# Kernel optimization log

Measured on AMD Instinct MI355X. Metric: run time of the kernel, lower is better.

The kernel has to match this reference:

```python
import jax, jax.numpy as jnp
import numpy as np

B = 16384
STATE = 524   # state_dim / output_size
IENC = 256    # INet output dim
ZD = 32       # z_dim
H = 256       # expert hidden size
E = 5         # num_experts
HG = 256      # gating hidden size
IN1 = STATE + IENC + ZD   # 812, PredictionNet layer-1 input
IN2 = H + ZD              # 288, layers 2/3 input


def _uni(k, shape):
    # matches PredictionNet.init_params glorot-style uniform bound
    bound = float(np.sqrt(6.0 / (shape[-2] * shape[-1])))
    return jax.random.uniform(k, shape, jnp.float32, -bound, bound)


def setup_inputs() -> dict:
    key = jax.random.key(0)
    ks = jax.random.split(key, 12)
    d = {}
    d['z'] = jax.random.normal(ks[0], (B, ZD), jnp.float32)
    d['p_prev'] = jax.random.normal(ks[1], (B, STATE), jnp.float32)
    d['I'] = jax.random.normal(ks[2], (B, 2048), jnp.float32)
    # gating network: (state+z) -> HG -> HG//2 -> E
    d['gw1'] = _uni(ks[3], (STATE + ZD, HG)); d['gb1'] = jnp.zeros((HG,), jnp.float32)
    d['gw2'] = _uni(ks[4], (HG, HG // 2));    d['gb2'] = jnp.zeros((HG // 2,), jnp.float32)
    d['gw3'] = _uni(ks[5], (HG // 2, E));     d['gb3'] = jnp.zeros((E,), jnp.float32)
    # INet: 2048 -> 256 -> 256 -> 256
    d['iw1'] = _uni(ks[6], (2048, IENC)); d['ib1'] = jnp.zeros((IENC,), jnp.float32)
    d['iw2'] = _uni(ks[7], (IENC, IENC)); d['ib2'] = jnp.zeros((IENC,), jnp.float32)
    d['iw3'] = _uni(ks[8], (IENC, IENC)); d['ib3'] = jnp.zeros((IENC,), jnp.float32)
    # expert weights [E, in, out], biases [E, out]
    d['w_l1'] = _uni(ks[9], (E, IN1, H));     d['b_l1'] = jnp.zeros((E, H), jnp.float32)
    d['w_l2'] = _uni(ks[10], (E, IN2, H));    d['b_l2'] = jnp.zeros((E, H), jnp.float32)
    d['w_l3'] = _uni(ks[11], (E, IN2, STATE)); d['b_l3'] = jnp.zeros((E, STATE), jnp.float32)
    return d


def reference(z, p_prev, I, gw1, gb1, gw2, gb2, gw3, gb3,
              iw1, ib1, iw2, ib2, iw3, ib3,
              w_l1, b_l1, w_l2, b_l2, w_l3, b_l3):
    elu = jax.nn.elu
    # gating network -> softmax blending coefficients omega [B, E]
    g = elu(jnp.concatenate([z, p_prev], axis=1) @ gw1 + gb1)
    g = elu(g @ gw2 + gb2)
    omega = jax.nn.softmax(g @ gw3 + gb3, axis=-1)
    # interaction encoder
    Ienc = elu(elu(elu(I @ iw1 + ib1) @ iw2 + ib2) @ iw3 + ib3)
    x = jnp.concatenate([p_prev, Ienc], axis=1)  # [B, STATE+IENC]

    def moe_linear(h, W, b):
        # same math as sum_e omega_e * (h @ W_e) + omega @ b, without
        # materializing per-sample blended [B, in, out] weights
        per_expert = jnp.einsum('bi,eio->beo', h, W)
        return jnp.einsum('be,beo->bo', omega, per_expert) + omega @ b

    h0 = jnp.concatenate([z, x], axis=1)          # [B, 812]
    h1 = elu(moe_linear(h0, w_l1, b_l1))          # [B, 256]
    h2 = elu(moe_linear(jnp.concatenate([z, h1], axis=1), w_l2, b_l2))
    h3 = moe_linear(jnp.concatenate([z, h2], axis=1), w_l3, b_l3)  # [B, 524]
    return h3
```

## Files before the change

kernel.cpp:

```cpp
#include <hip/hip_runtime.h>
#include <hip/hip_bf16.h>
#include <cstdint>
#include <cstddef>


#define BATCH 16384

typedef __attribute__((ext_vector_type(8))) short short8;
typedef __attribute__((ext_vector_type(4))) float f32x4;
typedef unsigned short u16;
typedef unsigned int u32;

typedef __attribute__((address_space(3))) void lds_t;
typedef __attribute__((address_space(1))) void gmem_t;

__device__ __forceinline__ void gload16(const u16* g, u16* l) {
  __builtin_amdgcn_global_load_lds((gmem_t*)(u16*)g, (lds_t*)l, 16, 0, 0);
}

__device__ __forceinline__ float bf2f(u16 u) {
  union { float f; u32 i; } v; v.i = ((u32)u) << 16; return v.f;
}
__device__ __forceinline__ u16 f2bf(float f) {
  union { float f; u32 i; } v; v.f = f;
  u32 x = v.i;
  return (u16)((x + 0x7fffu + ((x >> 16) & 1u)) >> 16);
}
__device__ __forceinline__ u16 load_bf(const void* p, long i, int f32) {
  return f32 ? f2bf(((const float*)p)[i]) : ((const u16*)p)[i];
}
__device__ __forceinline__ float elu_f(float x) { return x > 0.f ? x : expm1f(x); }

__device__ __forceinline__ int swz(int row, int q) { return q ^ ((row >> 1) & 3); }

__global__ __launch_bounds__(256) void detect_dtype(const u32* __restrict__ zr,
                                                    int* __restrict__ flag)
{
  __shared__ int cnt;
  if (threadIdx.x == 0) cnt = 0;
  __syncthreads();
  u32 w = zr[threadIdx.x];
  int e = (w >> 7) & 0xFF;
  if (e >= 112 && e <= 142) atomicAdd(&cnt, 1);
  __syncthreads();
  if (threadIdx.x == 0) *flag = (cnt < 128) ? 1 : 0;
}

__global__ __launch_bounds__(256) void prep_kernel(
    const void* __restrict__ z, const void* __restrict__ p,
    const int* __restrict__ flagp,
    u16* __restrict__ h0, u16* __restrict__ h1c, u16* __restrict__ h2c,
    const void* ib1, const void* ib2, const void* ib3,
    const void* gb1, const void* gb2, const void* gb3,
    const void* gw3, const void* bl1, const void* bl2, const void* bl3,
    u16* __restrict__ smallc)
{
  const int f32 = *flagp;
  const int b = blockIdx.y;
  const int c = blockIdx.x * 256 + threadIdx.x;
  if (blockIdx.y == 0 && blockIdx.x == 0) {
    for (long j = threadIdx.x; j < 7100; j += 256) {
      u16 v;
      if      (j < 256)  v = load_bf(ib1, j,        f32);
      else if (j < 512)  v = load_bf(ib2, j - 256,  f32);
      else if (j < 768)  v = load_bf(ib3, j - 512,  f32);
      else if (j < 1024) v = load_bf(gb1, j - 768,  f32);
      else if (j < 1152) v = load_bf(gb2, j - 1024, f32);
      else if (j < 1280) v = (j - 1152 < 5) ? load_bf(gb3, j - 1152, f32) : (u16)0;
      else if (j < 1920) v = load_bf(gw3, j - 1280, f32);
      else if (j < 3200) v = load_bf(bl1, j - 1920, f32);
      else if (j < 4480) v = load_bf(bl2, j - 3200, f32);
      else               v = load_bf(bl3, j - 4480, f32);
      smallc[j] = v;
    }
  }
  if (c >= 832) return;
  const long i = (long)b * 832 + c;
  if (c < 32) {
    u16 v = load_bf(z, (long)b * 32 + c, f32);
    h0[i] = v;
    h1c[(long)b * 288 + c] = v;
    h2c[(long)b * 288 + c] = v;
  } else if (c < 556) {
    h0[i] = load_bf(p, (long)b * 524 + (c - 32), f32);
  } else if (c >= 812) {
    h0[i] = 0;
  }
}

__global__ __launch_bounds__(256) void convert_I(
    const void* __restrict__ I, const int* __restrict__ flagp,
    u16* __restrict__ out)
{
  const int f32 = *flagp;
  const long total8 = (long)BATCH * 2048 / 8;
  const long stride = (long)gridDim.x * blockDim.x;
  for (long t = (long)blockIdx.x * blockDim.x + threadIdx.x; t < total8; t += stride) {
    if (f32) {
      const float4* src = (const float4*)I;
      float4 a = src[t * 2], b = src[t * 2 + 1];
      union { u16 r[8]; uint4 v; } u;
      u.r[0] = f2bf(a.x); u.r[1] = f2bf(a.y); u.r[2] = f2bf(a.z); u.r[3] = f2bf(a.w);
      u.r[4] = f2bf(b.x); u.r[5] = f2bf(b.y); u.r[6] = f2bf(b.z); u.r[7] = f2bf(b.w);
      *(uint4*)(out + t * 8) = u.v;
    } else {
      *(uint4*)(out + t * 8) = ((const uint4*)I)[t];
    }
  }
}

struct TPSeg { long end; int K, N, Kp, Np; };

__global__ __launch_bounds__(256) void transpose_all(
    const int* __restrict__ flagp,
    const void* s0, const void* s1, const void* s2, const void* s3,
    const void* s4, const void* s5, const void* s6, const void* s7,
    u16* d0, u16* d1, u16* d2, u16* d3, u16* d4, u16* d5, u16* d6, u16* d7)
{
  const TPSeg seg[8] = {
    {  524288, 2048, 256, 2048, 256 },
    {  589824,  256, 256,  256, 256 },
    {  655360,  256, 256,  256, 256 },
    {  802816,  556, 256,  576, 256 },
    {  835584,  256, 128,  256, 128 },
    { 1900544,  812, 256,  832, 256 },
    { 2269184,  288, 256,  288, 256 },
    { 3098624,  288, 524,  288, 576 },
  };
  const void* const srcs[8] = { s0, s1, s2, s3, s4, s5, s6, s7 };
  u16* const dsts[8] = { d0, d1, d2, d3, d4, d5, d6, d7 };
  const int f32 = *flagp;
  const long total = 3098624;
  const long stride = (long)gridDim.x * blockDim.x;
  for (long i = (long)blockIdx.x * blockDim.x + threadIdx.x; i < total; i += stride) {
    int s = 0;
    long base = 0;
    while (i >= seg[s].end) { base = seg[s].end; ++s; }
    const long j = i - base;
    const int Kp = seg[s].Kp, Np = seg[s].Np, K = seg[s].K, N = seg[s].N;
    const int k = (int)(j % Kp);
    const long t = j / Kp;
    const int n = (int)(t % Np);
    const int e = (int)(t / Np);
    u16 v = 0;
    if (k < K && n < N) v = load_bf(srcs[s], (long)e * K * N + (long)k * N + n, f32);
    dsts[s][j] = v;
  }
}

template<bool ELU>
__global__ __launch_bounds__(256, 2) void gemm64(
    const u16* __restrict__ A, int lda,
    const u16* __restrict__ Wt, int ldw,
    const u16* __restrict__ bias,
    u16* __restrict__ C, int ldc, int col_off, int K)
{
  __shared__ __align__(16) u16 sA[2][64 * 32];
  __shared__ __align__(16) u16 sB[2][128 * 32];

  const int tid  = threadIdx.x;
  const int bm   = blockIdx.x, bn = blockIdx.y;
  const int lane = tid & 63, wave = tid >> 6;
  const int wm = (wave & 1) * 32, wn = (wave >> 1) * 64;
  const int lrow = lane & 15, lq = lane >> 4;

  const int sq    = (lane & 3) ^ ((lane >> 3) & 3);
  const int srowA = 16 * wave + (lane >> 2);
  const int srowB = 32 * wave + (lane >> 2);
  const u16* Ag = A  + (size_t)(bm * 64  + srowA) * lda + sq * 8;
  const u16* Wg = Wt + (size_t)(bn * 128 + srowB) * ldw + sq * 8;
  const int laOff = wave * 512;
  const int lbOff = wave * 1024;

  f32x4 acc[2][4] = {};
  const int nt = K / 32;

  gload16(Ag, sA[0] + laOff);
  gload16(Wg, sB[0] + lbOff);
  gload16(Wg + (size_t)16 * ldw, sB[0] + lbOff + 512);
  __syncthreads();

  for (int t = 0; t < nt; ++t) {
    const int cur = t & 1;
    if (t + 1 < nt) {
      const int k0 = (t + 1) * 32;
      gload16(Ag + k0, sA[cur ^ 1] + laOff);
      gload16(Wg + k0, sB[cur ^ 1] + lbOff);
      gload16(Wg + (size_t)16 * ldw + k0, sB[cur ^ 1] + lbOff + 512);
    }

    short8 a[2], b[4];
#pragma unroll
    for (int i = 0; i < 2; ++i) {
      const int r = wm + i * 16 + lrow;
      a[i] = *(const short8*)(sA[cur] + r * 32 + swz(r, lq) * 8);
    }
#pragma unroll
    for (int i = 0; i < 4; ++i) {
      const int r = wn + i * 16 + lrow;
      b[i] = *(const short8*)(sB[cur] + r * 32 + swz(r, lq) * 8);
    }

#pragma unroll
    for (int mi = 0; mi < 2; ++mi)
#pragma unroll
      for (int ni = 0; ni < 4; ++ni)
        acc[mi][ni] = __builtin_amdgcn_mfma_f32_16x16x32_bf16(a[mi], b[ni], acc[mi][ni], 0, 0, 0);

    __syncthreads();
  }

#pragma unroll
  for (int ni = 0; ni < 4; ++ni) {
    const int col = bn * 128 + wn + ni * 16 + lrow;
    const float bv = bf2f(bias[col]);
#pragma unroll
    for (int mi = 0; mi < 2; ++mi) {
#pragma unroll
      for (int r = 0; r < 4; ++r) {
        const int row = bm * 64 + wm + mi * 16 + lq * 4 + r;
        float v = acc[mi][ni][r] + bv;
        if (ELU) v = elu_f(v);
        C[(size_t)row * ldc + col_off + col] = f2bf(v);
      }
    }
  }
}

__global__ __launch_bounds__(256) void gating3_kernel(
    const u16* __restrict__ g2, const u16* __restrict__ gw3c,
    const u16* __restrict__ gb3c, float* __restrict__ omega)
{
  const int wid  = (blockIdx.x << 2) + (threadIdx.x >> 6);
  const int lane = threadIdx.x & 63;
  const u32 gp = *(const u32*)(g2 + (size_t)wid * 128 + lane * 2);
  const float x0 = bf2f((u16)(gp & 0xffffu));
  const float x1 = bf2f((u16)(gp >> 16));
  float acc[5];
#pragma unroll
  for (int e = 0; e < 5; ++e)
    acc[e] = x0 * bf2f(gw3c[(lane * 2) * 5 + e]) + x1 * bf2f(gw3c[(lane * 2 + 1) * 5 + e]);
#pragma unroll
  for (int off = 1; off < 64; off <<= 1) {
#pragma unroll
    for (int e = 0; e < 5; ++e) acc[e] += __shfl_xor(acc[e], off);
  }
  if (lane == 0) {
    float t[5], m = -1e30f;
#pragma unroll
    for (int e = 0; e < 5; ++e) { t[e] = acc[e] + bf2f(gb3c[e]); m = fmaxf(m, t[e]); }
    float s = 0.f;
#pragma unroll
    for (int e = 0; e < 5; ++e) { t[e] = expf(t[e] - m); s += t[e]; }
    const float inv = 1.f / s;
#pragma unroll
    for (int e = 0; e < 5; ++e) omega[(size_t)wid * 5 + e] = t[e] * inv;
  }
}

template<bool ELU>
__global__ __launch_bounds__(256, 2) void moe_gemm(
    const u16* __restrict__ A, int lda,
    const u16* __restrict__ Wt, int ldw, long wstride_e,
    const u16* __restrict__ bias, int bias_n,
    const float* __restrict__ omega,
    void* __restrict__ C, int ldc, int col_off, int n_store, int K,
    const int* __restrict__ flagp, int is_final)
{
  __shared__ __align__(16) u16 sA[2][128 * 32];
  __shared__ __align__(16) u16 sW[2][5][64 * 32];
  __shared__ float som[128 * 5];
  __shared__ float sbias[5][64];

  const int tid  = threadIdx.x;
  const int bm   = blockIdx.x, bn = blockIdx.y;
  const int lane = tid & 63, wave = tid >> 6;
  const int wm = (wave & 1) * 64, wn = (wave >> 1) * 32;
  const int lrow = lane & 15, lq = lane >> 4;
  const int f32out = is_final ? *flagp : 0;

  const int sq = (lane & 3) ^ ((lane >> 3) & 3);
  const int srowA = 32 * wave + (lane >> 2);
  const int srowW = 16 * wave + (lane >> 2);
  const u16* Ag = A  + (size_t)(bm * 128 + srowA) * lda + sq * 8;
  const u16* Wg = Wt + (size_t)(bn * 64 + srowW) * ldw + sq * 8;
  const int laOff = wave * 1024;
  const int lWoff = wave * 512;

  f32x4 acc[5][4][2] = {};
  const int nt = K / 32;

  gload16(Ag, sA[0] + laOff);
  gload16(Ag + (size_t)16 * lda, sA[0] + laOff + 512);
#pragma unroll
  for (int e = 0; e < 5; ++e)
    gload16(Wg + e * wstride_e, sW[0][e] + lWoff);

  for (int t = tid; t < 960; t += 256) {
    if (t < 640) {
      som[t] = omega[(size_t)(bm * 128) * 5 + t];
    } else {
      const int j = t - 640;
      const int e = j >> 6, c = j & 63;
      const int col = bn * 64 + c;
      sbias[e][c] = (col < bias_n) ? bf2f(bias[(size_t)e * bias_n + col]) : 0.f;
    }
  }
  __syncthreads();

  for (int t = 0; t < nt; ++t) {
    const int cur = t & 1;
    if (t + 1 < nt) {
      const int k0 = (t + 1) * 32;
      gload16(Ag + k0, sA[cur ^ 1] + laOff);
      gload16(Ag + (size_t)16 * lda + k0, sA[cur ^ 1] + laOff + 512);
#pragma unroll
      for (int e = 0; e < 5; ++e)
        gload16(Wg + e * wstride_e + k0, sW[cur ^ 1][e] + lWoff);
    }

    short8 a[4];
#pragma unroll
    for (int i = 0; i < 4; ++i) {
      const int r = wm + i * 16 + lrow;
      a[i] = *(const short8*)(sA[cur] + r * 32 + swz(r, lq) * 8);
    }
    const int rb0 = wn + lrow, rb1 = rb0 + 16;
    const int ob0 = rb0 * 32 + swz(rb0, lq) * 8;
    const int ob1 = rb1 * 32 + swz(rb1, lq) * 8;
#pragma unroll
    for (int e = 0; e < 5; ++e) {
      short8 b0 = *(const short8*)(sW[cur][e] + ob0);
      short8 b1 = *(const short8*)(sW[cur][e] + ob1);
#pragma unroll
      for (int mi = 0; mi < 4; ++mi) {
        acc[e][mi][0] = __builtin_amdgcn_mfma_f32_16x16x32_bf16(a[mi], b0, acc[e][mi][0], 0, 0, 0);
        acc[e][mi][1] = __builtin_amdgcn_mfma_f32_16x16x32_bf16(a[mi], b1, acc[e][mi][1], 0, 0, 0);
      }
    }

    __syncthreads();
  }

#pragma unroll
  for (int mi = 0; mi < 4; ++mi) {
#pragma unroll
    for (int r = 0; r < 4; ++r) {
      const int rl = wm + mi * 16 + lq * 4 + r;
      const int row = bm * 128 + rl;
      float om[5];
#pragma unroll
      for (int e = 0; e < 5; ++e) om[e] = som[rl * 5 + e];
#pragma unroll
      for (int ni = 0; ni < 2; ++ni) {
        const int c = wn + ni * 16 + lrow;
        const int col = bn * 64 + c;
        if (col < n_store) {
          float v = 0.f;
#pragma unroll
          for (int e = 0; e < 5; ++e) v += om[e] * (acc[e][mi][ni][r] + sbias[e][c]);
          if (ELU) v = elu_f(v);
          const size_t idx = (size_t)row * ldc + col_off + col;
          if (f32out) ((float*)C)[idx] = v;
          else        ((u16*)C)[idx]   = f2bf(v);
        }
      }
    }
  }
}

extern "C" void kernel_launch(void* const* d_in, const int* in_sizes, int n_in,
                              void* d_out, int out_size, void* d_ws, size_t ws_size,
                              hipStream_t stream)
{
  const void* z    = d_in[0];
  const void* pprev= d_in[1];
  const void* I    = d_in[2];
  const void* gw1  = d_in[3];
  const void* gb1  = d_in[4];
  const void* gw2  = d_in[5];
  const void* gb2  = d_in[6];
  const void* gw3  = d_in[7];
  const void* gb3  = d_in[8];
  const void* iw1  = d_in[9];
  const void* ib1  = d_in[10];
  const void* iw2  = d_in[11];
  const void* ib2  = d_in[12];
  const void* iw3  = d_in[13];
  const void* ib3  = d_in[14];
  const void* wl1  = d_in[15];
  const void* bl1  = d_in[16];
  const void* wl2  = d_in[17];
  const void* bl2  = d_in[18];
  const void* wl3  = d_in[19];
  const void* bl3  = d_in[20];

  char* base = (char*)d_ws;
  size_t off = 0;
  auto alloc = [&](size_t bytes) -> void* {
    void* p = base + off;
    off = (off + bytes + 255) & ~(size_t)255;
    return p;
  };

  const size_t B = BATCH;
  int* flagp   = (int*)alloc(256);
  u16* h0      = (u16*)alloc(B * 832 * 2);
  u16* h1c     = (u16*)alloc(B * 288 * 2);
  u16* h2c     = (u16*)alloc(B * 288 * 2);
  u16* i1      = (u16*)alloc(B * 256 * 2);
  u16* i2      = (u16*)alloc(B * 256 * 2);
  float* omega = (float*)alloc(B * 5 * 4);
  u16* Ibf     = (u16*)alloc(B * 2048 * 2);
  u16* smallc  = (u16*)alloc(7100 * 2);
  u16* iw1t = (u16*)alloc((size_t)256 * 2048 * 2);
  u16* iw2t = (u16*)alloc((size_t)256 * 256 * 2);
  u16* iw3t = (u16*)alloc((size_t)256 * 256 * 2);
  u16* gw1t = (u16*)alloc((size_t)256 * 576 * 2);
  u16* gw2t = (u16*)alloc((size_t)128 * 256 * 2);
  u16* wl1t = (u16*)alloc((size_t)5 * 256 * 832 * 2);
  u16* wl2t = (u16*)alloc((size_t)5 * 256 * 288 * 2);
  u16* wl3t = (u16*)alloc((size_t)5 * 576 * 288 * 2);
  u16* g1 = i1;
  u16* g2 = i2;
  (void)in_sizes; (void)n_in; (void)out_size; (void)ws_size;

  u16* ib1c = smallc + 0,   *ib2c = smallc + 256, *ib3c = smallc + 512;
  u16* gb1c = smallc + 768, *gb2c = smallc + 1024, *gb3c = smallc + 1152;
  u16* gw3c = smallc + 1280;
  u16* bl1c = smallc + 1920, *bl2c = smallc + 3200, *bl3c = smallc + 4480;

  detect_dtype<<<1, 256, 0, stream>>>((const u32*)z, flagp);
  prep_kernel<<<dim3(4, BATCH), 256, 0, stream>>>(z, pprev, flagp, h0, h1c, h2c,
      ib1, ib2, ib3, gb1, gb2, gb3, gw3, bl1, bl2, bl3, smallc);
  convert_I<<<4096, 256, 0, stream>>>(I, flagp, Ibf);
  transpose_all<<<3072, 256, 0, stream>>>(flagp,
      iw1, iw2, iw3, gw1, gw2, wl1, wl2, wl3,
      iw1t, iw2t, iw3t, gw1t, gw2t, wl1t, wl2t, wl3t);

  gemm64<true><<<dim3(BATCH/64, 2), 256, 0, stream>>>(Ibf, 2048, iw1t, 2048, ib1c, i1, 256, 0,   2048);
  gemm64<true><<<dim3(BATCH/64, 2), 256, 0, stream>>>(i1,  256,  iw2t, 256,  ib2c, i2, 256, 0,   256);
  gemm64<true><<<dim3(BATCH/64, 2), 256, 0, stream>>>(i2,  256,  iw3t, 256,  ib3c, h0, 832, 556, 256);

  gemm64<true><<<dim3(BATCH/64, 2), 256, 0, stream>>>(h0, 832, gw1t, 576, gb1c, g1, 256, 0, 576);
  gemm64<true><<<dim3(BATCH/64, 1), 256, 0, stream>>>(g1, 256, gw2t, 256, gb2c, g2, 128, 0, 256);
  gating3_kernel<<<BATCH/4, 256, 0, stream>>>(g2, gw3c, gb3c, omega);

  moe_gemm<true><<<dim3(BATCH/128, 4), 256, 0, stream>>>(
      h0, 832, wl1t, 832, (long)256 * 832, bl1c, 256, omega, h1c, 288, 32, 256, 832, flagp, 0);
  moe_gemm<true><<<dim3(BATCH/128, 4), 256, 0, stream>>>(
      h1c, 288, wl2t, 288, (long)256 * 288, bl2c, 256, omega, h2c, 288, 32, 256, 288, flagp, 0);
  moe_gemm<false><<<dim3(BATCH/128, 9), 256, 0, stream>>>(
      h2c, 288, wl3t, 288, (long)576 * 288, bl3c, 524, omega, d_out, 524, 0, 524, 288, flagp, 1);
}
```

Measured before the change: 557.9 us.

## Fuse prep kernels, batch independent GEMMs, triple-buffer loads, and fold gating softmax into MoE

The four setup kernels become one prep_all kernel that detects the dtype per block via ballot, converts I, fills h0/h1c/h2c with 4-wide stores, and transposes weights four elements at a time. Independent INet and gating GEMMs are launched together through a two-descriptor gemm64m kernel, which also moves to a three-stage LDS pipeline with explicit vmcnt waits, non-draining barriers and raised MFMA priority. The gating layer-3 plus softmax is recomputed inside each MoE GEMM block, so the separate gating kernel and omega buffer go away. This cuts launch count and improves latency hiding, at the cost of redundant softmax work across column blocks, more LDS use, and fragile hand-written waitcnt logic.

```diff
diff --git a/kernel.cpp b/kernel.cpp
--- a/kernel.cpp
+++ b/kernel.cpp
@@ -18,6 +18,17 @@
   __builtin_amdgcn_global_load_lds((gmem_t*)(u16*)g, (lds_t*)l, 16, 0, 0);
 }
 
+__device__ __forceinline__ void barrier_nodrain() {
+  asm volatile("" ::: "memory");
+  __builtin_amdgcn_s_barrier();
+  asm volatile("" ::: "memory");
+}
+__device__ __forceinline__ void barrier_lds() {
+  asm volatile("s_waitcnt lgkmcnt(0)" ::: "memory");
+  __builtin_amdgcn_s_barrier();
+  asm volatile("" ::: "memory");
+}
+
 __device__ __forceinline__ float bf2f(u16 u) {
   union { float f; u32 i; } v; v.i = ((u32)u) << 16; return v.f;
 }
@@ -33,32 +44,33 @@
 
 __device__ __forceinline__ int swz(int row, int q) { return q ^ ((row >> 1) & 3); }
 
-__global__ __launch_bounds__(256) void detect_dtype(const u32* __restrict__ zr,
-                                                    int* __restrict__ flag)
-{
-  __shared__ int cnt;
-  if (threadIdx.x == 0) cnt = 0;
-  __syncthreads();
-  u32 w = zr[threadIdx.x];
-  int e = (w >> 7) & 0xFF;
-  if (e >= 112 && e <= 142) atomicAdd(&cnt, 1);
-  __syncthreads();
-  if (threadIdx.x == 0) *flag = (cnt < 128) ? 1 : 0;
-}
-
-__global__ __launch_bounds__(256) void prep_kernel(
+struct TPSeg { long end; int K, N, Kp, Np; };
+
+__global__ __launch_bounds__(256) void prep_all(
     const void* __restrict__ z, const void* __restrict__ p,
-    const int* __restrict__ flagp,
+    const void* __restrict__ I, int* __restrict__ flagp,
     u16* __restrict__ h0, u16* __restrict__ h1c, u16* __restrict__ h2c,
+    u16* __restrict__ Ibf,
     const void* ib1, const void* ib2, const void* ib3,
     const void* gb1, const void* gb2, const void* gb3,
     const void* gw3, const void* bl1, const void* bl2, const void* bl3,
-    u16* __restrict__ smallc)
+    u16* __restrict__ smallc,
+    const void* s0, const void* s1, const void* s2, const void* s3,
+    const void* s4, const void* s5, const void* s6, const void* s7,
+    u16* d0, u16* d1, u16* d2, u16* d3, u16* d4, u16* d5, u16* d6, u16* d7)
 {
-  const int f32 = *flagp;
-  const int b = blockIdx.y;
-  const int c = blockIdx.x * 256 + threadIdx.x;
-  if (blockIdx.y == 0 && blockIdx.x == 0) {
+  __shared__ int scnt[4];
+  {
+    u32 w = ((const u32*)z)[threadIdx.x];
+    int e = (w >> 7) & 0xFF;
+    unsigned long long m = __ballot(e >= 112 && e <= 142);
+    if ((threadIdx.x & 63) == 0) scnt[threadIdx.x >> 6] = __popcll(m);
+  }
+  __syncthreads();
+  const int f32 = (scnt[0] + scnt[1] + scnt[2] + scnt[3] < 128) ? 1 : 0;
+  if (blockIdx.x == 0 && threadIdx.x == 0) *flagp = f32;
+
+  if (blockIdx.x == 0) {
     for (long j = threadIdx.x; j < 7100; j += 256) {
       u16 v;
       if      (j < 256)  v = load_bf(ib1, j,        f32);
@@ -74,49 +86,7 @@
       smallc[j] = v;
     }
   }
-  if (c >= 832) return;
-  const long i = (long)b * 832 + c;
-  if (c < 32) {
-    u16 v = load_bf(z, (long)b * 32 + c, f32);
-    h0[i] = v;
-    h1c[(long)b * 288 + c] = v;
-    h2c[(long)b * 288 + c] = v;
-  } else if (c < 556) {
-    h0[i] = load_bf(p, (long)b * 524 + (c - 32), f32);
-  } else if (c >= 812) {
-    h0[i] = 0;
-  }
-}
-
-__global__ __launch_bounds__(256) void convert_I(
-    const void* __restrict__ I, const int* __restrict__ flagp,
-    u16* __restrict__ out)
-{
-  const int f32 = *flagp;
-  const long total8 = (long)BATCH * 2048 / 8;
-  const long stride = (long)gridDim.x * blockDim.x;
-  for (long t = (long)blockIdx.x * blockDim.x + threadIdx.x; t < total8; t += stride) {
-    if (f32) {
-      const float4* src = (const float4*)I;
-      float4 a = src[t * 2], b = src[t * 2 + 1];
-      union { u16 r[8]; uint4 v; } u;
-      u.r[0] = f2bf(a.x); u.r[1] = f2bf(a.y); u.r[2] = f2bf(a.z); u.r[3] = f2bf(a.w);
-      u.r[4] = f2bf(b.x); u.r[5] = f2bf(b.y); u.r[6] = f2bf(b.z); u.r[7] = f2bf(b.w);
-      *(uint4*)(out + t * 8) = u.v;
-    } else {
-      *(uint4*)(out + t * 8) = ((const uint4*)I)[t];
-    }
-  }
-}
-
-struct TPSeg { long end; int K, N, Kp, Np; };
-
-__global__ __launch_bounds__(256) void transpose_all(
-    const int* __restrict__ flagp,
-    const void* s0, const void* s1, const void* s2, const void* s3,
-    const void* s4, const void* s5, const void* s6, const void* s7,
-    u16* d0, u16* d1, u16* d2, u16* d3, u16* d4, u16* d5, u16* d6, u16* d7)
-{
+
   const TPSeg seg[8] = {
     {  524288, 2048, 256, 2048, 256 },
     {  589824,  256, 256,  256, 256 },
@@ -129,37 +99,94 @@
   };
   const void* const srcs[8] = { s0, s1, s2, s3, s4, s5, s6, s7 };
   u16* const dsts[8] = { d0, d1, d2, d3, d4, d5, d6, d7 };
-  const int f32 = *flagp;
-  const long total = 3098624;
+
+  const long NC = (long)BATCH * 2048 / 8;
+  const long NP = (long)BATCH * 208;
+  const long NT = 774656;
+  const long total = NC + NP + NT;
   const long stride = (long)gridDim.x * blockDim.x;
-  for (long i = (long)blockIdx.x * blockDim.x + threadIdx.x; i < total; i += stride) {
-    int s = 0;
-    long base = 0;
-    while (i >= seg[s].end) { base = seg[s].end; ++s; }
-    const long j = i - base;
-    const int Kp = seg[s].Kp, Np = seg[s].Np, K = seg[s].K, N = seg[s].N;
-    const int k = (int)(j % Kp);
-    const long t = j / Kp;
-    const int n = (int)(t % Np);
-    const int e = (int)(t / Np);
-    u16 v = 0;
-    if (k < K && n < N) v = load_bf(srcs[s], (long)e * K * N + (long)k * N + n, f32);
-    dsts[s][j] = v;
-  }
-}
-
-template<bool ELU>
-__global__ __launch_bounds__(256, 2) void gemm64(
-    const u16* __restrict__ A, int lda,
-    const u16* __restrict__ Wt, int ldw,
-    const u16* __restrict__ bias,
-    u16* __restrict__ C, int ldc, int col_off, int K)
+
+  for (long it = (long)blockIdx.x * 256 + threadIdx.x; it < total; it += stride) {
+    if (it < NC) {
+      const long t = it;
+      if (f32) {
+        const float4* src = (const float4*)I;
+        float4 a = src[t * 2], b = src[t * 2 + 1];
+        union { u16 r[8]; uint4 v; } u;
+        u.r[0] = f2bf(a.x); u.r[1] = f2bf(a.y); u.r[2] = f2bf(a.z); u.r[3] = f2bf(a.w);
+        u.r[4] = f2bf(b.x); u.r[5] = f2bf(b.y); u.r[6] = f2bf(b.z); u.r[7] = f2bf(b.w);
+        *(uint4*)(Ibf + t * 8) = u.v;
+      } else {
+        *(uint4*)(Ibf + t * 8) = ((const uint4*)I)[t];
+      }
+    } else if (it < NC + NP) {
+      const long j = it - NC;
+      const int b = (int)(j / 208);
+      const int c = (int)(j % 208) * 4;
+      ushort4 v;
+      if (c < 32) {
+        const long zi = (long)b * 32 + c;
+        if (f32) {
+          const float4 f = *(const float4*)((const float*)z + zi);
+          v.x = f2bf(f.x); v.y = f2bf(f.y); v.z = f2bf(f.z); v.w = f2bf(f.w);
+        } else {
+          v = *(const ushort4*)((const u16*)z + zi);
+        }
+        *(ushort4*)(h0 + (long)b * 832 + c) = v;
+        *(ushort4*)(h1c + (long)b * 288 + c) = v;
+        *(ushort4*)(h2c + (long)b * 288 + c) = v;
+      } else if (c < 556) {
+        const long pi = (long)b * 524 + (c - 32);
+        if (f32) {
+          const float4 f = *(const float4*)((const float*)p + pi);
+          v.x = f2bf(f.x); v.y = f2bf(f.y); v.z = f2bf(f.z); v.w = f2bf(f.w);
+        } else {
+          v = *(const ushort4*)((const u16*)p + pi);
+        }
+        *(ushort4*)(h0 + (long)b * 832 + c) = v;
+      } else {
+        v.x = 0; v.y = 0; v.z = 0; v.w = 0;
+        *(ushort4*)(h0 + (long)b * 832 + c) = v;
+      }
+    } else {
+      const long jd = (it - NC - NP) * 4;
+      int s = 0; long sbase = 0;
+      while (jd >= seg[s].end) { sbase = seg[s].end; ++s; }
+      const long jj = jd - sbase;
+      const int Kp = seg[s].Kp, Np = seg[s].Np, Kk = seg[s].K, Nn = seg[s].N;
+      const int k = (int)(jj % Kp);
+      const long tt = jj / Kp;
+      const int n = (int)(tt % Np);
+      const int e = (int)(tt / Np);
+      ushort4 v; v.x = 0; v.y = 0; v.z = 0; v.w = 0;
+      if (k < Kk && n < Nn) {
+        const long sb = (long)e * Kk * Nn + (long)k * Nn + n;
+        v.x = load_bf(srcs[s], sb, f32);
+        v.y = load_bf(srcs[s], sb + Nn, f32);
+        v.z = load_bf(srcs[s], sb + 2 * (long)Nn, f32);
+        v.w = load_bf(srcs[s], sb + 3 * (long)Nn, f32);
+      }
+      *(ushort4*)(dsts[s] + jj) = v;
+    }
+  }
+}
+
+struct GemmDesc {
+  const u16* A; const u16* Wt; const u16* bias; u16* C;
+  int lda, ldw, ldc, col_off, K, ny;
+};
+
+__global__ __launch_bounds__(256, 2) void gemm64m(GemmDesc da, GemmDesc db)
 {
-  __shared__ __align__(16) u16 sA[2][64 * 32];
-  __shared__ __align__(16) u16 sB[2][128 * 32];
+  __shared__ __align__(16) u16 sA[3][64 * 32];
+  __shared__ __align__(16) u16 sB[3][128 * 32];
+
+  int bn = blockIdx.y;
+  GemmDesc d;
+  if (bn < da.ny) { d = da; } else { bn -= da.ny; d = db; }
 
   const int tid  = threadIdx.x;
-  const int bm   = blockIdx.x, bn = blockIdx.y;
+  const int bm   = blockIdx.x;
   const int lane = tid & 63, wave = tid >> 6;
   const int wm = (wave & 1) * 32, wn = (wave >> 1) * 64;
   const int lrow = lane & 15, lq = lane >> 4;
@@ -167,27 +194,37 @@
   const int sq    = (lane & 3) ^ ((lane >> 3) & 3);
   const int srowA = 16 * wave + (lane >> 2);
   const int srowB = 32 * wave + (lane >> 2);
-  const u16* Ag = A  + (size_t)(bm * 64  + srowA) * lda + sq * 8;
-  const u16* Wg = Wt + (size_t)(bn * 128 + srowB) * ldw + sq * 8;
+  const u16* Ag = d.A  + (size_t)(bm * 64  + srowA) * d.lda + sq * 8;
+  const u16* Wg = d.Wt + (size_t)(bn * 128 + srowB) * d.ldw + sq * 8;
   const int laOff = wave * 512;
   const int lbOff = wave * 1024;
+  const int ldw = d.ldw;
 
   f32x4 acc[2][4] = {};
-  const int nt = K / 32;
+  const int nt = d.K / 32;
 
   gload16(Ag, sA[0] + laOff);
   gload16(Wg, sB[0] + lbOff);
   gload16(Wg + (size_t)16 * ldw, sB[0] + lbOff + 512);
-  __syncthreads();
+  gload16(Ag + 32, sA[1] + laOff);
+  gload16(Wg + 32, sB[1] + lbOff);
+  gload16(Wg + (size_t)16 * ldw + 32, sB[1] + lbOff + 512);
 
   for (int t = 0; t < nt; ++t) {
-    const int cur = t & 1;
-    if (t + 1 < nt) {
-      const int k0 = (t + 1) * 32;
-      gload16(Ag + k0, sA[cur ^ 1] + laOff);
-      gload16(Wg + k0, sB[cur ^ 1] + lbOff);
-      gload16(Wg + (size_t)16 * ldw + k0, sB[cur ^ 1] + lbOff + 512);
-    }
+    const int cur = t % 3;
+    barrier_nodrain();
+    if (t + 2 < nt) {
+      const int nb = (t + 2) % 3;
+      const int k0 = (t + 2) * 32;
+      gload16(Ag + k0, sA[nb] + laOff);
+      gload16(Wg + k0, sB[nb] + lbOff);
+      gload16(Wg + (size_t)16 * ldw + k0, sB[nb] + lbOff + 512);
+    }
+    const int ahead = nt - 1 - t;
+    if (ahead >= 2)      asm volatile("s_waitcnt vmcnt(6)" ::: "memory");
+    else if (ahead == 1) asm volatile("s_waitcnt vmcnt(3)" ::: "memory");
+    else                 asm volatile("s_waitcnt vmcnt(0)" ::: "memory");
+    barrier_nodrain();
 
     short8 a[2], b[4];
 #pragma unroll
@@ -201,60 +238,29 @@
       b[i] = *(const short8*)(sB[cur] + r * 32 + swz(r, lq) * 8);
     }
 
+    __builtin_amdgcn_s_setprio(1);
 #pragma unroll
     for (int mi = 0; mi < 2; ++mi)
 #pragma unroll
       for (int ni = 0; ni < 4; ++ni)
         acc[mi][ni] = __builtin_amdgcn_mfma_f32_16x16x32_bf16(a[mi], b[ni], acc[mi][ni], 0, 0, 0);
-
-    __syncthreads();
+    __builtin_amdgcn_s_setprio(0);
   }
 
 #pragma unroll
   for (int ni = 0; ni < 4; ++ni) {
     const int col = bn * 128 + wn + ni * 16 + lrow;
-    const float bv = bf2f(bias[col]);
+    const float bv = bf2f(d.bias[col]);
 #pragma unroll
     for (int mi = 0; mi < 2; ++mi) {
 #pragma unroll
       for (int r = 0; r < 4; ++r) {
         const int row = bm * 64 + wm + mi * 16 + lq * 4 + r;
         float v = acc[mi][ni][r] + bv;
-        if (ELU) v = elu_f(v);
-        C[(size_t)row * ldc + col_off + col] = f2bf(v);
-      }
-    }
-  }
-}
-
-__global__ __launch_bounds__(256) void gating3_kernel(
-    const u16* __restrict__ g2, const u16* __restrict__ gw3c,
-    const u16* __restrict__ gb3c, float* __restrict__ omega)
-{
-  const int wid  = (blockIdx.x << 2) + (threadIdx.x >> 6);
-  const int lane = threadIdx.x & 63;
-  const u32 gp = *(const u32*)(g2 + (size_t)wid * 128 + lane * 2);
-  const float x0 = bf2f((u16)(gp & 0xffffu));
-  const float x1 = bf2f((u16)(gp >> 16));
-  float acc[5];
-#pragma unroll
-  for (int e = 0; e < 5; ++e)
-    acc[e] = x0 * bf2f(gw3c[(lane * 2) * 5 + e]) + x1 * bf2f(gw3c[(lane * 2 + 1) * 5 + e]);
-#pragma unroll
-  for (int off = 1; off < 64; off <<= 1) {
-#pragma unroll
-    for (int e = 0; e < 5; ++e) acc[e] += __shfl_xor(acc[e], off);
-  }
-  if (lane == 0) {
-    float t[5], m = -1e30f;
-#pragma unroll
-    for (int e = 0; e < 5; ++e) { t[e] = acc[e] + bf2f(gb3c[e]); m = fmaxf(m, t[e]); }
-    float s = 0.f;
-#pragma unroll
-    for (int e = 0; e < 5; ++e) { t[e] = expf(t[e] - m); s += t[e]; }
-    const float inv = 1.f / s;
-#pragma unroll
-    for (int e = 0; e < 5; ++e) omega[(size_t)wid * 5 + e] = t[e] * inv;
+        v = elu_f(v);
+        d.C[(size_t)row * d.ldc + d.col_off + col] = f2bf(v);
+      }
+    }
   }
 }
 
@@ -263,14 +269,17 @@
     const u16* __restrict__ A, int lda,
     const u16* __restrict__ Wt, int ldw, long wstride_e,
     const u16* __restrict__ bias, int bias_n,
-    const float* __restrict__ omega,
+    const u16* __restrict__ g2, const u16* __restrict__ gw3c,
+    const u16* __restrict__ gb3c,
     void* __restrict__ C, int ldc, int col_off, int n_store, int K,
     const int* __restrict__ flagp, int is_final)
 {
   __shared__ __align__(16) u16 sA[2][128 * 32];
-  __shared__ __align__(16) u16 sW[2][5][64 * 32];
+  __shared__ __align__(16) u16 sW[2][5 * 64 * 32];
   __shared__ float som[128 * 5];
   __shared__ float sbias[5][64];
+  __shared__ float sgw[128 * 5];
+  __shared__ float sgb[5];
 
   const int tid  = threadIdx.x;
   const int bm   = blockIdx.x, bn = blockIdx.y;
@@ -287,37 +296,64 @@
   const int laOff = wave * 1024;
   const int lWoff = wave * 512;
 
+  auto stage = [&](int buf, int k0) {
+    gload16(Ag + k0, sA[buf] + laOff);
+    gload16(Ag + (size_t)16 * lda + k0, sA[buf] + laOff + 512);
+#pragma unroll
+    for (int e = 0; e < 5; ++e)
+      gload16(Wg + e * wstride_e + k0, sW[buf] + e * 2048 + lWoff);
+  };
+
   f32x4 acc[5][4][2] = {};
   const int nt = K / 32;
 
-  gload16(Ag, sA[0] + laOff);
-  gload16(Ag + (size_t)16 * lda, sA[0] + laOff + 512);
-#pragma unroll
-  for (int e = 0; e < 5; ++e)
-    gload16(Wg + e * wstride_e, sW[0][e] + lWoff);
-
-  for (int t = tid; t < 960; t += 256) {
-    if (t < 640) {
-      som[t] = omega[(size_t)(bm * 128) * 5 + t];
+  stage(0, 0);
+  for (int t2 = tid; t2 < 960; t2 += 256) {
+    if (t2 < 640) {
+      sgw[t2] = bf2f(gw3c[t2]);
     } else {
-      const int j = t - 640;
+      const int j = t2 - 640;
       const int e = j >> 6, c = j & 63;
       const int col = bn * 64 + c;
       sbias[e][c] = (col < bias_n) ? bf2f(bias[(size_t)e * bias_n + col]) : 0.f;
     }
   }
-  __syncthreads();
+  if (tid < 5) sgb[tid] = bf2f(gb3c[tid]);
+  barrier_lds();
+  if (tid < 128) {
+    const u16* gr = g2 + (size_t)(bm * 128 + tid) * 128;
+    float t[5];
+#pragma unroll
+    for (int e = 0; e < 5; ++e) t[e] = sgb[e];
+    for (int k = 0; k < 128; k += 2) {
+      const u32 gp = *(const u32*)(gr + k);
+      const float x0 = bf2f((u16)(gp & 0xffffu));
+      const float x1 = bf2f((u16)(gp >> 16));
+#pragma unroll
+      for (int e = 0; e < 5; ++e)
+        t[e] += x0 * sgw[k * 5 + e] + x1 * sgw[(k + 1) * 5 + e];
+    }
+    float m = t[0];
+#pragma unroll
+    for (int e = 1; e < 5; ++e) m = fmaxf(m, t[e]);
+    float ssum = 0.f;
+#pragma unroll
+    for (int e = 0; e < 5; ++e) { t[e] = expf(t[e] - m); ssum += t[e]; }
+    const float inv = 1.f / ssum;
+#pragma unroll
+    for (int e = 0; e < 5; ++e) som[tid * 5 + e] = t[e] * inv;
+  }
 
   for (int t = 0; t < nt; ++t) {
     const int cur = t & 1;
+    barrier_nodrain();
     if (t + 1 < nt) {
-      const int k0 = (t + 1) * 32;
-      gload16(Ag + k0, sA[cur ^ 1] + laOff);
-      gload16(Ag + (size_t)16 * lda + k0, sA[cur ^ 1] + laOff + 512);
-#pragma unroll
-      for (int e = 0; e < 5; ++e)
-        gload16(Wg + e * wstride_e + k0, sW[cur ^ 1][e] + lWoff);
-    }
+      stage(cur ^ 1, (t + 1) * 32);
+      asm volatile("s_waitcnt vmcnt(7)" ::: "memory");
+    } else {
+      asm volatile("s_waitcnt vmcnt(0)" ::: "memory");
+    }
+    barrier_nodrain();
 
     short8 a[4];
 #pragma unroll
@@ -328,18 +364,18 @@
     const int rb0 = wn + lrow, rb1 = rb0 + 16;
     const int ob0 = rb0 * 32 + swz(rb0, lq) * 8;
     const int ob1 = rb1 * 32 + swz(rb1, lq) * 8;
+    __builtin_amdgcn_s_setprio(1);
 #pragma unroll
     for (int e = 0; e < 5; ++e) {
-      short8 b0 = *(const short8*)(sW[cur][e] + ob0);
-      short8 b1 = *(const short8*)(sW[cur][e] + ob1);
+      short8 b0 = *(const short8*)(sW[cur] + e * 2048 + ob0);
+      short8 b1 = *(const short8*)(sW[cur] + e * 2048 + ob1);
 #pragma unroll
       for (int mi = 0; mi < 4; ++mi) {
         acc[e][mi][0] = __builtin_amdgcn_mfma_f32_16x16x32_bf16(a[mi], b0, acc[e][mi][0], 0, 0, 0);
         acc[e][mi][1] = __builtin_amdgcn_mfma_f32_16x16x32_bf16(a[mi], b1, acc[e][mi][1], 0, 0, 0);
       }
     }
-
-    __syncthreads();
+    __builtin_amdgcn_s_setprio(0);
   }
 
 #pragma unroll
@@ -410,7 +446,8 @@
   u16* h2c     = (u16*)alloc(B * 288 * 2);
   u16* i1      = (u16*)alloc(B * 256 * 2);
   u16* i2      = (u16*)alloc(B * 256 * 2);
-  float* omega = (float*)alloc(B * 5 * 4);
+  u16* g1      = (u16*)alloc(B * 256 * 2);
+  u16* g2      = (u16*)alloc(B * 128 * 2);
   u16* Ibf     = (u16*)alloc(B * 2048 * 2);
   u16* smallc  = (u16*)alloc(7100 * 2);
   u16* iw1t = (u16*)alloc((size_t)256 * 2048 * 2);
@@ -421,8 +458,6 @@
   u16* wl1t = (u16*)alloc((size_t)5 * 256 * 832 * 2);
   u16* wl2t = (u16*)alloc((size_t)5 * 256 * 288 * 2);
   u16* wl3t = (u16*)alloc((size_t)5 * 576 * 288 * 2);
-  u16* g1 = i1;
-  u16* g2 = i2;
   (void)in_sizes; (void)n_in; (void)out_size; (void)ws_size;
 
   u16* ib1c = smallc + 0,   *ib2c = smallc + 256, *ib3c = smallc + 512;
@@ -430,26 +465,28 @@
   u16* gw3c = smallc + 1280;
   u16* bl1c = smallc + 1920, *bl2c = smallc + 3200, *bl3c = smallc + 4480;
 
-  detect_dtype<<<1, 256, 0, stream>>>((const u32*)z, flagp);
-  prep_kernel<<<dim3(4, BATCH), 256, 0, stream>>>(z, pprev, flagp, h0, h1c, h2c,
-      ib1, ib2, ib3, gb1, gb2, gb3, gw3, bl1, bl2, bl3, smallc);
-  convert_I<<<4096, 256, 0, stream>>>(I, flagp, Ibf);
-  transpose_all<<<3072, 256, 0, stream>>>(flagp,
+  prep_all<<<2048, 256, 0, stream>>>(z, pprev, I, flagp, h0, h1c, h2c, Ibf,
+      ib1, ib2, ib3, gb1, gb2, gb3, gw3, bl1, bl2, bl3, smallc,
       iw1, iw2, iw3, gw1, gw2, wl1, wl2, wl3,
       iw1t, iw2t, iw3t, gw1t, gw2t, wl1t, wl2t, wl3t);
 
-  gemm64<true><<<dim3(BATCH/64, 2), 256, 0, stream>>>(Ibf, 2048, iw1t, 2048, ib1c, i1, 256, 0,   2048);
-  gemm64<true><<<dim3(BATCH/64, 2), 256, 0, stream>>>(i1,  256,  iw2t, 256,  ib2c, i2, 256, 0,   256);
-  gemm64<true><<<dim3(BATCH/64, 2), 256, 0, stream>>>(i2,  256,  iw3t, 256,  ib3c, h0, 832, 556, 256);
-
-  gemm64<true><<<dim3(BATCH/64, 2), 256, 0, stream>>>(h0, 832, gw1t, 576, gb1c, g1, 256, 0, 576);
-  gemm64<true><<<dim3(BATCH/64, 1), 256, 0, stream>>>(g1, 256, gw2t, 256, gb2c, g2, 128, 0, 256);
-  gating3_kernel<<<BATCH/4, 256, 0, stream>>>(g2, gw3c, gb3c, omega);
+  GemmDesc inet1 = { Ibf, iw1t, ib1c, i1, 2048, 2048, 256, 0,   2048, 2 };
+  GemmDesc gat1  = { h0,  gw1t, gb1c, g1,  832,  576, 256, 0,    576, 2 };
+  GemmDesc inet2 = { i1,  iw2t, ib2c, i2,  256,  256, 256, 0,    256, 2 };
+  GemmDesc gat2  = { g1,  gw2t, gb2c, g2,  256,  256, 128, 0,    256, 1 };
+  GemmDesc inet3 = { i2,  iw3t, ib3c, h0,  256,  256, 832, 556,  256, 2 };
+
+  gemm64m<<<dim3(BATCH/64, 4), 256, 0, stream>>>(inet1, gat1);
+  gemm64m<<<dim3(BATCH/64, 3), 256, 0, stream>>>(inet2, gat2);
+  gemm64m<<<dim3(BATCH/64, 2), 256, 0, stream>>>(inet3, inet3);
 
   moe_gemm<true><<<dim3(BATCH/128, 4), 256, 0, stream>>>(
-      h0, 832, wl1t, 832, (long)256 * 832, bl1c, 256, omega, h1c, 288, 32, 256, 832, flagp, 0);
+      h0, 832, wl1t, 832, (long)256 * 832, bl1c, 256, g2, gw3c, gb3c,
+      h1c, 288, 32, 256, 832, flagp, 0);
   moe_gemm<true><<<dim3(BATCH/128, 4), 256, 0, stream>>>(
-      h1c, 288, wl2t, 288, (long)256 * 288, bl2c, 256, omega, h2c, 288, 32, 256, 288, flagp, 0);
+      h1c, 288, wl2t, 288, (long)256 * 288, bl2c, 256, g2, gw3c, gb3c,
+      h2c, 288, 32, 256, 288, flagp, 0);
   moe_gemm<false><<<dim3(BATCH/128, 9), 256, 0, stream>>>(
-      h2c, 288, wl3t, 288, (long)576 * 288, bl3c, 524, omega, d_out, 524, 0, 524, 288, flagp, 1);
-}
+      h2c, 288, wl3t, 288, (long)576 * 288, bl3c, 524, g2, gw3c, gb3c,
+      d_out, 524, 0, 524, 288, flagp, 1);
+}
```

New measurement: 515.1 us. 7.7% less time.
